# Performance work log

Measured on AMD Instinct MI355X. Metric: run time of the kernel, lower is better.

## Reference

```python
import jax, jax.numpy as jnp
import numpy as np

B = 16384
IN_DIM = 28 * 28
HID = 768
NUM_EXPERTS = 8
NUM_CLASSES = 10
H_PHASOR = 32          # phasor bank harmonics -> 2*H features
DELTA0 = 7.0
DECAY = 0.7            # spiking attention leak
THETA = 1.0
K_WINNERS = 5
TOP_K_ROUTE = 2
TRAITS = (0.6, 0.6, 0.5, 0.5, 0.4)


def setup_inputs() -> dict:
    key = jax.random.key(0)
    ks = jax.random.split(key, 16)
    s = 0.02
    return {
        "x": jax.random.normal(ks[0], (B, 28, 28), jnp.float32),
        "W_in": jax.random.normal(ks[1], (IN_DIM, HID), jnp.float32) * s,
        "b_in": jnp.zeros((HID,), jnp.float32),
        "W_ph": jax.random.normal(ks[2], (2 * H_PHASOR, HID), jnp.float32) * s,
        "b_ph": jnp.zeros((HID,), jnp.float32),
        "W_gate": jax.random.normal(ks[3], (HID, NUM_EXPERTS), jnp.float32) * s,
        "b_gate": jnp.zeros((NUM_EXPERTS,), jnp.float32),
        "W_exp": jax.random.normal(ks[4], (NUM_EXPERTS, HID, HID), jnp.float32) * s,
        "b_exp": jnp.zeros((NUM_EXPERTS, HID), jnp.float32),
        "W_th": jax.random.normal(ks[5], (HID, NUM_EXPERTS), jnp.float32) * s,
        "b_th": jnp.zeros((NUM_EXPERTS,), jnp.float32),
        "W_pm": jax.random.normal(ks[6], (5, NUM_EXPERTS), jnp.float32) * s,
        "b_pm": jnp.zeros((NUM_EXPERTS,), jnp.float32),
        "W_out": jax.random.normal(ks[7], (HID, NUM_CLASSES), jnp.float32) * s,
        "b_out": jnp.zeros((NUM_CLASSES,), jnp.float32),
    }


def reference(x, W_in, b_in, W_ph, b_ph, W_gate, b_gate, W_exp, b_exp,
              W_th, b_th, W_pm, b_pm, W_out, b_out):
    Bn = x.shape[0]
    x_flat = x.reshape((Bn, -1))
    proj = x_flat @ W_in + b_in                                  # [B, HID]

    # Phasor bank on per-sample mean activation: sin/cos at H harmonics
    x_mean = jnp.mean(proj, axis=-1)                             # [B]
    freqs = DELTA0 * jnp.arange(1, H_PHASOR + 1, dtype=proj.dtype)
    phase = x_mean[:, None] * freqs[None, :]                     # [B, H]
    feats = jnp.concatenate([jnp.sin(phase), jnp.cos(phase)], -1)  # [B, 2H]
    enhanced = proj + feats @ W_ph + b_ph                        # [B, HID]

    # Top-K index selection feeding gather/scatter spiking attention
    V = enhanced.shape[-1]
    K = min(32, V)
    topk_idx = jax.lax.top_k(enhanced, K)[1].astype(jnp.int32)   # [B, K]
    w = DECAY ** jnp.arange(K, dtype=enhanced.dtype)             # decaying drive

    def gains_fn(idx):
        v = jnp.zeros((V,), enhanced.dtype).at[idx].add(w)       # scatter-add
        vals, widx = jax.lax.top_k(v, K_WINNERS)                 # k-WTA
        return jnp.ones((V,), enhanced.dtype).at[widx].add(vals / THETA)

    gains = jax.vmap(gains_fn)(topk_idx)                         # [B, V]
    attended = enhanced * gains

    # Personality bias + thalamic bias (thalamic_scale = 1.0)
    traits = jnp.asarray(TRAITS, dtype=enhanced.dtype)
    pbias = traits @ W_pm + b_pm                                 # [E]
    thal = jnp.mean(attended, axis=0) @ W_th + b_th              # [E]

    # MoE retrieval core: gate -> top-k softmax route -> combine experts
    gate_logits = attended @ W_gate + b_gate + pbias[None] + thal[None]  # [B, E]
    gvals, gidx = jax.lax.top_k(gate_logits, TOP_K_ROUTE)        # [B, k]
    gw = jax.nn.softmax(gvals, axis=-1)                          # [B, k]
    exp_out = jnp.einsum('bh,ehd->bed', attended, W_exp) + b_exp[None]   # [B, E, HID]
    sel = jnp.take_along_axis(exp_out, gidx[:, :, None], axis=1)  # [B, k, HID]
    context = jnp.sum(gw[:, :, None] * sel, axis=1)              # [B, HID]

    return context @ W_out + b_out                               # [B, classes]
```

## Files before the change

### kernel.cpp

```cpp
#include <hip/hip_runtime.h>
#include <hip/hip_bf16.h>
#include <cstddef>

#define BATCH 16384
#define IND   784
#define HID   768
#define NEXP  8
#define KT13  13

typedef short bf16x8 __attribute__((ext_vector_type(8)));
typedef float f32x4  __attribute__((ext_vector_type(4)));
typedef unsigned short ushort_t;

#define GLD16(g, l)                                                            \
  __builtin_amdgcn_global_load_lds(                                            \
      (const __attribute__((address_space(1))) unsigned int*)(g),              \
      (__attribute__((address_space(3))) unsigned int*)(l), 16, 0, 0)

__global__ __launch_bounds__(256) void k_wtrans(const float* __restrict__ Wexp,
                                                __hip_bfloat16* __restrict__ Wt)
{
  __shared__ float tile[32][33];
  const int e = blockIdx.z;
  const int h0 = blockIdx.x * 32, d0 = blockIdx.y * 32;
  const int tx = threadIdx.x & 31, ty = threadIdx.x >> 5;
  const float* src = Wexp + ((size_t)e * HID + h0) * HID + d0;
  #pragma unroll
  for (int i = 0; i < 4; i++)
    tile[ty + 8 * i][tx] = src[(size_t)(ty + 8 * i) * HID + tx];
  __syncthreads();
  __hip_bfloat16* dst = Wt + ((size_t)e * HID + d0) * HID + h0;
  #pragma unroll
  for (int i = 0; i < 4; i++)
    dst[(size_t)(ty + 8 * i) * HID + tx] = __float2bfloat16(tile[tx][ty + 8 * i]);
}

__device__ inline ushort_t bf16_rne(float f) {
  union { float f; unsigned u; } v; v.f = f;
  unsigned r = v.u + 0x7fffu + ((v.u >> 16) & 1u);
  return (ushort_t)(r >> 16);
}
__device__ inline float bf16_to_f(ushort_t h) {
  union { unsigned u; float f; } v; v.u = ((unsigned)h) << 16;
  return v.f;
}

__global__ __launch_bounds__(256) void k_packA(const float* __restrict__ x,
                                               ushort_t* __restrict__ Ahi,
                                               ushort_t* __restrict__ Alo)
{
  const int kt = blockIdx.x, mt = blockIdx.y;
  const size_t tbase = ((size_t)mt * KT13 + kt) * 8192;
  const int kb = kt * 64;
  #pragma unroll
  for (int i = 0; i < 4; i++) {
    int id = i * 256 + threadIdx.x;
    int r = id >> 3, c = id & 7;
    int row = mt * 128 + r;
    int k0 = kb + c * 8;
    float v[8];
    if (k0 + 8 <= IND) {
      const float4* p = reinterpret_cast<const float4*>(x + (size_t)row * IND + k0);
      float4 a = p[0], b = p[1];
      v[0] = a.x; v[1] = a.y; v[2] = a.z; v[3] = a.w;
      v[4] = b.x; v[5] = b.y; v[6] = b.z; v[7] = b.w;
    } else {
      #pragma unroll
      for (int j = 0; j < 8; j++) v[j] = (k0 + j < IND) ? x[(size_t)row * IND + k0 + j] : 0.f;
    }
    ushort_t hi[8], lo[8];
    #pragma unroll
    for (int j = 0; j < 8; j++) {
      hi[j] = bf16_rne(v[j]);
      lo[j] = bf16_rne(v[j] - bf16_to_f(hi[j]));
    }
    size_t dst = tbase + (size_t)r * 64 + ((c ^ (r & 7)) * 8);
    *reinterpret_cast<uint4*>(Ahi + dst) = *reinterpret_cast<uint4*>(hi);
    *reinterpret_cast<uint4*>(Alo + dst) = *reinterpret_cast<uint4*>(lo);
  }
}

__global__ __launch_bounds__(256) void k_packB(const float* __restrict__ W,
                                               ushort_t* __restrict__ Bhi,
                                               ushort_t* __restrict__ Blo)
{
  const int kt = blockIdx.x, nt = blockIdx.y;
  const size_t tbase = ((size_t)nt * KT13 + kt) * 8192;
  const int kb = kt * 64;
  #pragma unroll
  for (int i = 0; i < 4; i++) {
    int id = i * 256 + threadIdx.x;
    int r = id >> 3, c = id & 7;
    int n = nt * 128 + r;
    int k0 = kb + c * 8;
    float v[8];
    #pragma unroll
    for (int j = 0; j < 8; j++)
      v[j] = (k0 + j < IND) ? W[(size_t)(k0 + j) * HID + n] : 0.f;
    ushort_t hi[8], lo[8];
    #pragma unroll
    for (int j = 0; j < 8; j++) {
      hi[j] = bf16_rne(v[j]);
      lo[j] = bf16_rne(v[j] - bf16_to_f(hi[j]));
    }
    size_t dst = tbase + (size_t)r * 64 + ((c ^ (r & 7)) * 8);
    *reinterpret_cast<uint4*>(Bhi + dst) = *reinterpret_cast<uint4*>(hi);
    *reinterpret_cast<uint4*>(Blo + dst) = *reinterpret_cast<uint4*>(lo);
  }
}

__global__ __launch_bounds__(256, 2) void k_proj2(const ushort_t* __restrict__ Ahi,
                                                  const ushort_t* __restrict__ Alo,
                                                  const ushort_t* __restrict__ Bhi,
                                                  const ushort_t* __restrict__ Blo,
                                                  const float* __restrict__ bias,
                                                  float* __restrict__ out)
{
  __shared__ __align__(16) ushort_t lds[4 * 8192];
  const int tid = threadIdx.x, lane = tid & 63, w = tid >> 6;
  const int mt = blockIdx.y, nt = blockIdx.x;
  const int m0 = (w >> 1) * 64, n0 = (w & 1) * 64;
  const int l15 = lane & 15, g = lane >> 4;

  f32x4 acc[4][4];
  #pragma unroll
  for (int i = 0; i < 4; i++)
    #pragma unroll
    for (int j = 0; j < 4; j++) acc[i][j] = (f32x4){0.f, 0.f, 0.f, 0.f};

  const size_t abase = (size_t)mt * KT13 * 8192;
  const size_t bbase = (size_t)nt * KT13 * 8192;

  for (int kt = 0; kt < KT13; kt++) {
    __syncthreads();
    const ushort_t* srcs[4] = { Ahi + abase + (size_t)kt * 8192,
                                Alo + abase + (size_t)kt * 8192,
                                Bhi + bbase + (size_t)kt * 8192,
                                Blo + bbase + (size_t)kt * 8192 };
    #pragma unroll
    for (int buf = 0; buf < 4; buf++) {
      #pragma unroll
      for (int i = 0; i < 4; i++) {
        int off = w * 2048 + i * 512 + lane * 8;
        GLD16(srcs[buf] + off, &lds[buf * 8192 + w * 2048 + i * 512]);
      }
    }
    asm volatile("s_waitcnt vmcnt(0)");
    __syncthreads();
    #pragma unroll
    for (int ks = 0; ks < 2; ks++) {
      bf16x8 ah[4], al[4], bh[4], bl[4];
      #pragma unroll
      for (int i = 0; i < 4; i++) {
        int ca = ((4 * ks + g) ^ (l15 & 7)) * 8;
        int ra = m0 + 16 * i + l15;
        ah[i] = *reinterpret_cast<const bf16x8*>(&lds[0 * 8192 + ra * 64 + ca]);
        al[i] = *reinterpret_cast<const bf16x8*>(&lds[1 * 8192 + ra * 64 + ca]);
        int rb = n0 + 16 * i + l15;
        bh[i] = *reinterpret_cast<const bf16x8*>(&lds[2 * 8192 + rb * 64 + ca]);
        bl[i] = *reinterpret_cast<const bf16x8*>(&lds[3 * 8192 + rb * 64 + ca]);
      }
      #pragma unroll
      for (int i = 0; i < 4; i++)
        #pragma unroll
        for (int j = 0; j < 4; j++) {
          acc[i][j] = __builtin_amdgcn_mfma_f32_16x16x32_bf16(ah[i], bh[j], acc[i][j], 0, 0, 0);
          acc[i][j] = __builtin_amdgcn_mfma_f32_16x16x32_bf16(ah[i], bl[j], acc[i][j], 0, 0, 0);
          acc[i][j] = __builtin_amdgcn_mfma_f32_16x16x32_bf16(al[i], bh[j], acc[i][j], 0, 0, 0);
        }
    }
  }
  #pragma unroll
  for (int i = 0; i < 4; i++) {
    #pragma unroll
    for (int q = 0; q < 4; q++) {
      int m = mt * 128 + m0 + 16 * i + g * 4 + q;
      #pragma unroll
      for (int j = 0; j < 4; j++) {
        int n = nt * 128 + n0 + 16 * j + l15;
        out[(size_t)m * HID + n] = acc[i][j][q] + bias[n];
      }
    }
  }
}

__global__ __launch_bounds__(256) void k_mean(const float* __restrict__ proj,
                                              float* __restrict__ means)
{
  const int t = threadIdx.x, lane = t & 63, w = t >> 6;
  const int row = blockIdx.x * 4 + w;
  const float* p = proj + (size_t)row * HID;
  float s = 0.f;
  #pragma unroll
  for (int j = 0; j < 12; j++) s += p[lane + 64 * j];
  #pragma unroll
  for (int off = 32; off; off >>= 1) s += __shfl_xor(s, off);
  if (lane == 0) means[row] = s * (1.0f / 768.0f);
}

__global__ __launch_bounds__(256) void k_phasor(const float* __restrict__ means,
                                                const float* __restrict__ Wph,
                                                const float* __restrict__ bph,
                                                float* __restrict__ enh)
{
  __shared__ float Fs[64][132];
  __shared__ float Ws[64][128];
  const int t  = threadIdx.x;
  const int bm = blockIdx.y * 128, bn = blockIdx.x * 128;
  {
    const int r = t >> 1;
    const float mn = means[bm + r];
    if ((t & 1) == 0) {
      #pragma unroll
      for (int j = 0; j < 32; j++) Fs[j][r] = sinf(mn * (7.0f * (j + 1)));
    } else {
      #pragma unroll
      for (int j = 0; j < 32; j++) Fs[32 + j][r] = cosf(mn * (7.0f * (j + 1)));
    }
  }
  #pragma unroll
  for (int i = 0; i < 8; i++) {
    int f4 = i * 256 + t;
    int k = f4 >> 5, n4 = (f4 & 31) * 4;
    *reinterpret_cast<float4*>(&Ws[k][n4]) =
        *reinterpret_cast<const float4*>(Wph + (size_t)k * HID + bn + n4);
  }
  __syncthreads();

  const int m0 = (t >> 4) * 8, n0 = (t & 15) * 8;
  float acc[8][8];
  #pragma unroll
  for (int i = 0; i < 8; i++)
    #pragma unroll
    for (int j = 0; j < 8; j++) acc[i][j] = 0.f;
  #pragma unroll 4
  for (int k = 0; k < 64; k++) {
    float a[8], b[8];
    *reinterpret_cast<float4*>(&a[0]) = *reinterpret_cast<const float4*>(&Fs[k][m0]);
    *reinterpret_cast<float4*>(&a[4]) = *reinterpret_cast<const float4*>(&Fs[k][m0 + 4]);
    *reinterpret_cast<float4*>(&b[0]) = *reinterpret_cast<const float4*>(&Ws[k][n0]);
    *reinterpret_cast<float4*>(&b[4]) = *reinterpret_cast<const float4*>(&Ws[k][n0 + 4]);
    #pragma unroll
    for (int i = 0; i < 8; i++)
      #pragma unroll
      for (int j = 0; j < 8; j++) acc[i][j] = fmaf(a[i], b[j], acc[i][j]);
  }
  float bl[8];
  #pragma unroll
  for (int j = 0; j < 8; j++) bl[j] = bph[bn + n0 + j];
  #pragma unroll
  for (int i = 0; i < 8; i++) {
    float* rowp = enh + (size_t)(bm + m0 + i) * HID + bn + n0;
    float4 p0 = *reinterpret_cast<float4*>(rowp);
    float4 p1 = *reinterpret_cast<float4*>(rowp + 4);
    p0.x += acc[i][0] + bl[0]; p0.y += acc[i][1] + bl[1];
    p0.z += acc[i][2] + bl[2]; p0.w += acc[i][3] + bl[3];
    p1.x += acc[i][4] + bl[4]; p1.y += acc[i][5] + bl[5];
    p1.z += acc[i][6] + bl[6]; p1.w += acc[i][7] + bl[7];
    *reinterpret_cast<float4*>(rowp)     = p0;
    *reinterpret_cast<float4*>(rowp + 4) = p1;
  }
}

__global__ __launch_bounds__(256) void k_attend(const float* __restrict__ enh,
                                                const float* __restrict__ Wg,
                                                __hip_bfloat16* __restrict__ attb,
                                                float* __restrict__ glog,
                                                float* __restrict__ partials)
{
  __shared__ float WgT[8][768];
  __shared__ float cs[4][768];
  const int t = threadIdx.x, lane = t & 63, w = t >> 6;
  for (int i = t; i < 768 * 8; i += 256) { int c = i >> 3, e = i & 7; WgT[e][c] = Wg[i]; }
  for (int i = t; i < 4 * 768; i += 256) cs[i / 768][i % 768] = 0.f;
  __syncthreads();

  for (int rr = 0; rr < 8; ++rr) {
    const int row = blockIdx.x * 32 + rr * 4 + w;
    const float* er = enh + (size_t)row * HID;
    float o[12], s[12];
    #pragma unroll
    for (int j = 0; j < 12; j++) { o[j] = er[lane + 64 * j]; s[j] = o[j]; }

    int wc[5];
    #pragma unroll
    for (int k = 0; k < 5; k++) {
      float v = -3.4e38f; int c = 0x7fffffff;
      #pragma unroll
      for (int j = 0; j < 12; j++)
        if (s[j] > v) { v = s[j]; c = lane + 64 * j; }
      #pragma unroll
      for (int off = 32; off; off >>= 1) {
        float ov = __shfl_xor(v, off); int oc = __shfl_xor(c, off);
        if (ov > v || (ov == v && oc < c)) { v = ov; c = oc; }
      }
      wc[k] = c;
      if (lane == (c & 63)) {
        #pragma unroll
        for (int j = 0; j < 12; j++) if (j == (c >> 6)) s[j] = -3.4e38f;
      }
    }

    float a[12];
    #pragma unroll
    for (int j = 0; j < 12; j++) a[j] = o[j];
    float wv = 1.0f;
    #pragma unroll
    for (int k = 0; k < 5; k++) {
      int c = wc[k];
      if (lane == (c & 63)) {
        #pragma unroll
        for (int j = 0; j < 12; j++) if (j == (c >> 6)) a[j] = o[j] * (1.0f + wv);
      }
      wv *= 0.7f;
    }
    #pragma unroll
    for (int j = 0; j < 12; j++)
      attb[(size_t)row * HID + lane + 64 * j] = __float2bfloat16(a[j]);
    #pragma unroll
    for (int j = 0; j < 12; j++) cs[w][lane + 64 * j] += a[j];

    float p[8];
    #pragma unroll
    for (int e = 0; e < 8; e++) p[e] = 0.f;
    #pragma unroll
    for (int j = 0; j < 12; j++) {
      int c = lane + 64 * j;
      #pragma unroll
      for (int e = 0; e < 8; e++) p[e] = fmaf(a[j], WgT[e][c], p[e]);
    }
    #pragma unroll
    for (int e = 0; e < 8; e++) {
      #pragma unroll
      for (int off = 32; off; off >>= 1) p[e] += __shfl_xor(p[e], off);
    }
    if (lane == 0) {
      #pragma unroll
      for (int e = 0; e < 8; e++) glog[(size_t)row * 8 + e] = p[e];
    }
  }
  __syncthreads();
  for (int i = t; i < 768; i += 256)
    partials[(size_t)blockIdx.x * 768 + i] = cs[0][i] + cs[1][i] + cs[2][i] + cs[3][i];
}

__global__ void k_thal(const float* __restrict__ partials,
                       const float* __restrict__ Wth, const float* __restrict__ bth,
                       const float* __restrict__ Wpm, const float* __restrict__ bpm,
                       const float* __restrict__ bgate, float* __restrict__ add8)
{
  __shared__ float cm[768];
  __shared__ float th[8];
  const int t = threadIdx.x;
  float s = 0.f;
  #pragma unroll 8
  for (int b = 0; b < 512; b++) s += partials[(size_t)b * 768 + t];
  cm[t] = s * (1.0f / 16384.0f);
  __syncthreads();
  if (t < 256) {
    int e = t >> 5, l = t & 31;
    float ps = 0.f;
    for (int c = l; c < 768; c += 32) ps = fmaf(cm[c], Wth[(size_t)c * 8 + e], ps);
    #pragma unroll
    for (int off = 16; off; off >>= 1) ps += __shfl_xor(ps, off);
    if (l == 0) th[e] = ps + bth[e];
  }
  __syncthreads();
  if (t < 8) {
    const float TR[5] = {0.6f, 0.6f, 0.5f, 0.5f, 0.4f};
    float pb = bpm[t];
    #pragma unroll
    for (int i = 0; i < 5; i++) pb = fmaf(TR[i], Wpm[i * 8 + t], pb);
    add8[t] = th[t] + pb + bgate[t];
  }
}

__global__ __launch_bounds__(256) void k_route(const float* __restrict__ glog,
                                               const float* __restrict__ add8,
                                               float* __restrict__ rw,
                                               unsigned char* __restrict__ re,
                                               int* __restrict__ counts)
{
  __shared__ float a8[8];
  __shared__ int lc[8];
  const int t = threadIdx.x;
  if (t < 8) { a8[t] = add8[t]; lc[t] = 0; }
  __syncthreads();
  const int row = blockIdx.x * 256 + t;
  const float4* gp = reinterpret_cast<const float4*>(glog + (size_t)row * 8);
  float4 g0 = gp[0], g1 = gp[1];
  float l[8] = { g0.x + a8[0], g0.y + a8[1], g0.z + a8[2], g0.w + a8[3],
                 g1.x + a8[4], g1.y + a8[5], g1.z + a8[6], g1.w + a8[7] };
  float v0 = l[0], v1 = -3.4e38f; int i0 = 0, i1 = 0;
  #pragma unroll
  for (int e = 1; e < 8; e++) {
    if (l[e] > v0)      { v1 = v0; i1 = i0; v0 = l[e]; i0 = e; }
    else if (l[e] > v1) { v1 = l[e]; i1 = e; }
  }
  float ex = expf(v1 - v0);
  float inv = 1.0f / (1.0f + ex);
  rw[row * 2] = inv; rw[row * 2 + 1] = ex * inv;
  re[row * 2] = (unsigned char)i0; re[row * 2 + 1] = (unsigned char)i1;
  atomicAdd(&lc[i0], 1); atomicAdd(&lc[i1], 1);
  __syncthreads();
  if (t < 8) atomicAdd(&counts[t], lc[t]);
}

__global__ void k_prefix(const int* __restrict__ counts, int* __restrict__ meta)
{
  if (threadIdx.x == 0) {
    int o = 0, tt = 0;
    for (int e = 0; e < 8; e++) {
      meta[e] = o; meta[9 + e] = tt; meta[19 + e] = o;
      o += counts[e]; tt += (counts[e] + 127) >> 7;
    }
    meta[8] = o; meta[17] = tt; meta[18] = tt;
  }
}

__global__ __launch_bounds__(256) void k_scatter(const unsigned char* __restrict__ re,
                                                 int* __restrict__ meta,
                                                 int* __restrict__ perm,
                                                 int* __restrict__ inv)
{
  __shared__ int lc[8], base[8];
  const int t = threadIdx.x;
  if (t < 8) lc[t] = 0;
  __syncthreads();
  const int row = blockIdx.x * 256 + t;
  const int e0 = re[row * 2], e1 = re[row * 2 + 1];
  const int p0 = atomicAdd(&lc[e0], 1);
  const int p1 = atomicAdd(&lc[e1], 1);
  __syncthreads();
  if (t < 8) base[t] = atomicAdd(&meta[19 + t], lc[t]);
  __syncthreads();
  const int s0 = base[e0] + p0;
  const int s1 = base[e1] + p1;
  perm[s0] = row * 2;     inv[row * 2]     = s0;
  perm[s1] = row * 2 + 1; inv[row * 2 + 1] = s1;
}

__global__ __launch_bounds__(256) void k_expert(const unsigned short* __restrict__ attb,
                                                const unsigned short* __restrict__ Wt,
                                                const float* __restrict__ bexp,
                                                const float* __restrict__ rw,
                                                const int* __restrict__ perm,
                                                const int* __restrict__ meta,
                                                ushort_t* __restrict__ ctxP)
{
  if ((int)blockIdx.x >= meta[18]) return;
  __shared__ __align__(16) unsigned short AsBs[2 * 128 * 64];
  __shared__ int rid[128];
  __shared__ float gws[128];
  __shared__ float bxs[128];
  unsigned short* As = AsBs;
  unsigned short* Bs = AsBs + 128 * 64;

  const int* tst = meta + 9;
  const int tb = blockIdx.x;
  int e = 0;
  #pragma unroll
  for (int i = 1; i < 8; i++) if (tb >= tst[i]) e = i;
  const int tix  = tb - tst[e];
  const int off  = meta[e];
  const int cnt  = meta[e + 1] - off;
  const int rbase = off + tix * 128;
  const int vcnt  = min(128, cnt - tix * 128);
  const int tid = threadIdx.x;
  const int nb  = blockIdx.y * 128;

  if (tid < 128) {
    if (tid < vcnt) {
      int p = perm[rbase + tid];
      rid[tid] = p >> 1; gws[tid] = rw[p];
    } else {
      rid[tid] = 0; gws[tid] = 0.f;
    }
    bxs[tid] = bexp[(size_t)e * HID + nb + tid];
  }
  __syncthreads();

  const int lane = tid & 63, w = tid >> 6;
  const int m0 = (w >> 1) * 64, n0 = (w & 1) * 64;
  const int l15 = lane & 15, g = lane >> 4;
  const unsigned short* wbase = Wt + ((size_t)e * HID + nb) * HID;

  f32x4 acc[4][4];
  #pragma unroll
  for (int i = 0; i < 4; i++)
    #pragma unroll
    for (int j = 0; j < 4; j++) acc[i][j] = (f32x4){0.f, 0.f, 0.f, 0.f};

  for (int kb = 0; kb < HID; kb += 64) {
    __syncthreads();
    #pragma unroll
    for (int i = 0; i < 4; i++) {
      int id = i * 256 + tid;
      int r = id >> 3, c = id & 7;
      int sc = (c ^ (r & 7)) * 8;
      GLD16(attb + (size_t)rid[r] * HID + kb + sc, As + (i * 256 + w * 64) * 8);
      GLD16(wbase + (size_t)r * HID + kb + sc,      Bs + (i * 256 + w * 64) * 8);
    }
    asm volatile("s_waitcnt vmcnt(0)");
    __syncthreads();
    #pragma unroll
    for (int ks = 0; ks < 2; ks++) {
      bf16x8 af[4], bfr[4];
      #pragma unroll
      for (int i = 0; i < 4; i++) {
        int ca = (((4 * ks + g) ^ (l15 & 7)) * 8);
        af[i]  = *reinterpret_cast<const bf16x8*>(As + (m0 + 16 * i + l15) * 64 + ca);
        bfr[i] = *reinterpret_cast<const bf16x8*>(Bs + (n0 + 16 * i + l15) * 64 + ca);
      }
      #pragma unroll
      for (int i = 0; i < 4; i++)
        #pragma unroll
        for (int j = 0; j < 4; j++)
          acc[i][j] = __builtin_amdgcn_mfma_f32_16x16x32_bf16(af[i], bfr[j], acc[i][j], 0, 0, 0);
    }
  }

  unsigned short* Cs = AsBs;
  __syncthreads();
  #pragma unroll
  for (int i = 0; i < 4; i++) {
    #pragma unroll
    for (int q = 0; q < 4; q++) {
      int m = m0 + 16 * i + g * 4 + q;
      float gwv = gws[m];
      #pragma unroll
      for (int j = 0; j < 4; j++) {
        int n = n0 + 16 * j + l15;
        Cs[m * 128 + n] = bf16_rne(gwv * (acc[i][j][q] + bxs[n]));
      }
    }
  }
  __syncthreads();
  #pragma unroll
  for (int c = 0; c < 8; c++) {
    int r = w * 32 + c * 4 + (lane >> 4);
    if (r < vcnt) {
      uint4 v = *reinterpret_cast<const uint4*>(Cs + r * 128 + l15 * 8);
      *reinterpret_cast<uint4*>(ctxP + (size_t)(rbase + r) * HID + nb + l15 * 8) = v;
    }
  }
}

__global__ __launch_bounds__(256) void k_out(const ushort_t* __restrict__ ctxP,
                                             const int* __restrict__ inv,
                                             const float* __restrict__ Wout,
                                             const float* __restrict__ bout,
                                             float* __restrict__ out)
{
  __shared__ float wT[10][768];
  const int t = threadIdx.x, lane = t & 63, w = t >> 6;
  for (int i = t; i < 7680; i += 256) { int cl = i / 768, d = i - cl * 768; wT[cl][d] = Wout[(size_t)d * 10 + cl]; }
  __syncthreads();
  for (int rr = 0; rr < 8; ++rr) {
    const int row = blockIdx.x * 32 + rr * 4 + w;
    const int s0 = inv[row * 2], s1 = inv[row * 2 + 1];
    const ushort_t* p0 = ctxP + (size_t)s0 * HID;
    const ushort_t* p1 = ctxP + (size_t)s1 * HID;
    float cd[12];
    #pragma unroll
    for (int j = 0; j < 12; j++)
      cd[j] = bf16_to_f(p0[lane + 64 * j]) + bf16_to_f(p1[lane + 64 * j]);
    float p[10];
    #pragma unroll
    for (int cl = 0; cl < 10; cl++) {
      float ps = 0.f;
      #pragma unroll
      for (int j = 0; j < 12; j++) ps = fmaf(cd[j], wT[cl][lane + 64 * j], ps);
      #pragma unroll
      for (int off = 32; off; off >>= 1) ps += __shfl_xor(ps, off);
      p[cl] = ps;
    }
    if (lane == 0) {
      #pragma unroll
      for (int cl = 0; cl < 10; cl++) out[(size_t)row * 10 + cl] = p[cl] + bout[cl];
    }
  }
}

extern "C" void kernel_launch(void* const* d_in, const int* in_sizes, int n_in,
                              void* d_out, int out_size, void* d_ws, size_t ws_size,
                              hipStream_t stream)
{
  const float* x     = (const float*)d_in[0];
  const float* W_in  = (const float*)d_in[1];
  const float* b_in  = (const float*)d_in[2];
  const float* W_ph  = (const float*)d_in[3];
  const float* b_ph  = (const float*)d_in[4];
  const float* W_g   = (const float*)d_in[5];
  const float* b_g   = (const float*)d_in[6];
  const float* W_exp = (const float*)d_in[7];
  const float* b_exp = (const float*)d_in[8];
  const float* W_th  = (const float*)d_in[9];
  const float* b_th  = (const float*)d_in[10];
  const float* W_pm  = (const float*)d_in[11];
  const float* b_pm  = (const float*)d_in[12];
  const float* W_out = (const float*)d_in[13];
  const float* b_out = (const float*)d_in[14];
  float* out = (float*)d_out;

  char* ws = (char*)d_ws;
  size_t off = 0;
  float* enh   = (float*)(ws + off); off += (size_t)BATCH * HID * 4;
  char*  aliasbase = ws + off;
  off += (size_t)BATCH * HID * 4;
  __hip_bfloat16* attb = (__hip_bfloat16*)(ws + off); off += (size_t)BATCH * HID * 2;
  __hip_bfloat16* Wt   = (__hip_bfloat16*)(ws + off); off += (size_t)NEXP * HID * HID * 2;
  float* glog     = (float*)(ws + off); off += (size_t)BATCH * 8 * 4;
  float* partials = (float*)(ws + off); off += (size_t)512 * 768 * 4;
  float* means    = (float*)(ws + off); off += (size_t)BATCH * 4;
  float* add8     = (float*)(ws + off); off += 256;
  float* rw       = (float*)(ws + off); off += (size_t)BATCH * 2 * 4;
  unsigned char* re = (unsigned char*)(ws + off); off += (size_t)BATCH * 2;
  int* counts = (int*)(ws + off); off += 256;
  int* meta   = (int*)(ws + off); off += 256;
  int* perm   = (int*)(ws + off); off += (size_t)BATCH * 2 * 4;
  int* invp   = (int*)(ws + off); off += (size_t)BATCH * 2 * 4;
  ushort_t* Bhi = (ushort_t*)(ws + off); off += (size_t)KT13 * 64 * HID * 2;
  ushort_t* Blo = (ushort_t*)(ws + off); off += (size_t)KT13 * 64 * HID * 2;
  ushort_t* Ahi = (ushort_t*)aliasbase;
  ushort_t* Alo = (ushort_t*)(aliasbase + (size_t)BATCH * KT13 * 64 * 2);
  ushort_t* ctxP = (ushort_t*)enh;

  hipMemsetAsync(counts, 0, 32, stream);
  k_wtrans<<<dim3(24, 24, 8), 256, 0, stream>>>(W_exp, Wt);
  k_packA <<<dim3(13, 128),   256, 0, stream>>>(x, Ahi, Alo);
  k_packB <<<dim3(13, 6),     256, 0, stream>>>(W_in, Bhi, Blo);
  k_proj2 <<<dim3(6, 128),    256, 0, stream>>>(Ahi, Alo, Bhi, Blo, b_in, enh);
  k_mean  <<<4096,            256, 0, stream>>>(enh, means);
  k_phasor<<<dim3(6, 128),    256, 0, stream>>>(means, W_ph, b_ph, enh);
  k_attend<<<512,             256, 0, stream>>>(enh, W_g, attb, glog, partials);
  k_thal  <<<1,               768, 0, stream>>>(partials, W_th, b_th, W_pm, b_pm, b_g, add8);
  k_route <<<64,              256, 0, stream>>>(glog, add8, rw, re, counts);
  k_prefix<<<1,                64, 0, stream>>>(counts, meta);
  k_scatter<<<64,             256, 0, stream>>>(re, meta, perm, invp);
  k_expert<<<dim3(264, 6),    256, 0, stream>>>((const unsigned short*)attb, (const unsigned short*)Wt,
                                                b_exp, rw, perm, meta, ctxP);
  k_out   <<<512,             256, 0, stream>>>(ctxP, invp, W_out, b_out, out);
}
```

Baseline: 340.8 us.

## Fuse row-mean into projection GEMM, drop LDS staging, double-buffer expert GEMM

The projection GEMM now reads its pre-packed, unswizzled bf16 hi/lo tiles straight from global memory into registers instead of staging them through LDS. It also uses a remapped 1D block order and emits per-row partial sums, so the separate mean kernel disappears and the phasor kernel reduces 12 partials itself. The expert GEMM gains two-stage double-buffered global-to-LDS loads, and its grid is transposed so the N tiles of one expert tile run back to back. Workspace is re-aliased so attb and Wt overlay the packed A buffers, and k_wtrans moves after the projection. Direct global fragment loads may raise memory traffic, and the aliasing requires the new launch order.

```diff
diff --git a/kernel.cpp b/kernel.cpp
--- a/kernel.cpp
+++ b/kernel.cpp
@@ -74,7 +74,7 @@
       hi[j] = bf16_rne(v[j]);
       lo[j] = bf16_rne(v[j] - bf16_to_f(hi[j]));
     }
-    size_t dst = tbase + (size_t)r * 64 + ((c ^ (r & 7)) * 8);
+    size_t dst = tbase + (size_t)r * 64 + c * 8;
     *reinterpret_cast<uint4*>(Ahi + dst) = *reinterpret_cast<uint4*>(hi);
     *reinterpret_cast<uint4*>(Alo + dst) = *reinterpret_cast<uint4*>(lo);
   }
@@ -103,22 +103,24 @@
       hi[j] = bf16_rne(v[j]);
       lo[j] = bf16_rne(v[j] - bf16_to_f(hi[j]));
     }
-    size_t dst = tbase + (size_t)r * 64 + ((c ^ (r & 7)) * 8);
+    size_t dst = tbase + (size_t)r * 64 + c * 8;
     *reinterpret_cast<uint4*>(Bhi + dst) = *reinterpret_cast<uint4*>(hi);
     *reinterpret_cast<uint4*>(Blo + dst) = *reinterpret_cast<uint4*>(lo);
   }
 }
 
-__global__ __launch_bounds__(256, 2) void k_proj2(const ushort_t* __restrict__ Ahi,
-                                                  const ushort_t* __restrict__ Alo,
-                                                  const ushort_t* __restrict__ Bhi,
-                                                  const ushort_t* __restrict__ Blo,
-                                                  const float* __restrict__ bias,
-                                                  float* __restrict__ out)
-{
-  __shared__ __align__(16) ushort_t lds[4 * 8192];
+__global__ __launch_bounds__(256) void k_proj3(const ushort_t* __restrict__ Ahi,
+                                               const ushort_t* __restrict__ Alo,
+                                               const ushort_t* __restrict__ Bhi,
+                                               const ushort_t* __restrict__ Blo,
+                                               const float* __restrict__ bias,
+                                               float* __restrict__ out,
+                                               float* __restrict__ pm)
+{
+  const int bid = blockIdx.x;
+  const int sid = (bid & 7) * 96 + (bid >> 3);
+  const int mt = sid / 6, nt = sid - 6 * mt;
   const int tid = threadIdx.x, lane = tid & 63, w = tid >> 6;
-  const int mt = blockIdx.y, nt = blockIdx.x;
   const int m0 = (w >> 1) * 64, n0 = (w & 1) * 64;
   const int l15 = lane & 15, g = lane >> 4;
 
@@ -132,44 +134,36 @@
   const size_t bbase = (size_t)nt * KT13 * 8192;
 
   for (int kt = 0; kt < KT13; kt++) {
-    __syncthreads();
-    const ushort_t* srcs[4] = { Ahi + abase + (size_t)kt * 8192,
-                                Alo + abase + (size_t)kt * 8192,
-                                Bhi + bbase + (size_t)kt * 8192,
-                                Blo + bbase + (size_t)kt * 8192 };
-    #pragma unroll
-    for (int buf = 0; buf < 4; buf++) {
+    const ushort_t* ath = Ahi + abase + (size_t)kt * 8192;
+    const ushort_t* atl = Alo + abase + (size_t)kt * 8192;
+    const ushort_t* bth = Bhi + bbase + (size_t)kt * 8192;
+    const ushort_t* btl = Blo + bbase + (size_t)kt * 8192;
+    #pragma unroll
+    for (int ks = 0; ks < 2; ks++) {
+      bf16x8 ah[4], al[4], bh[4], blv[4];
       #pragma unroll
       for (int i = 0; i < 4; i++) {
-        int off = w * 2048 + i * 512 + lane * 8;
-        GLD16(srcs[buf] + off, &lds[buf * 8192 + w * 2048 + i * 512]);
-      }
-    }
-    asm volatile("s_waitcnt vmcnt(0)");
-    __syncthreads();
-    #pragma unroll
-    for (int ks = 0; ks < 2; ks++) {
-      bf16x8 ah[4], al[4], bh[4], bl[4];
-      #pragma unroll
-      for (int i = 0; i < 4; i++) {
-        int ca = ((4 * ks + g) ^ (l15 & 7)) * 8;
-        int ra = m0 + 16 * i + l15;
-        ah[i] = *reinterpret_cast<const bf16x8*>(&lds[0 * 8192 + ra * 64 + ca]);
-        al[i] = *reinterpret_cast<const bf16x8*>(&lds[1 * 8192 + ra * 64 + ca]);
-        int rb = n0 + 16 * i + l15;
-        bh[i] = *reinterpret_cast<const bf16x8*>(&lds[2 * 8192 + rb * 64 + ca]);
-        bl[i] = *reinterpret_cast<const bf16x8*>(&lds[3 * 8192 + rb * 64 + ca]);
+        int oa = (m0 + 16 * i + l15) * 64 + (4 * ks + g) * 8;
+        ah[i]  = *reinterpret_cast<const bf16x8*>(ath + oa);
+        al[i]  = *reinterpret_cast<const bf16x8*>(atl + oa);
+        int ob = (n0 + 16 * i + l15) * 64 + (4 * ks + g) * 8;
+        bh[i]  = *reinterpret_cast<const bf16x8*>(bth + ob);
+        blv[i] = *reinterpret_cast<const bf16x8*>(btl + ob);
       }
       #pragma unroll
       for (int i = 0; i < 4; i++)
         #pragma unroll
         for (int j = 0; j < 4; j++) {
-          acc[i][j] = __builtin_amdgcn_mfma_f32_16x16x32_bf16(ah[i], bh[j], acc[i][j], 0, 0, 0);
-          acc[i][j] = __builtin_amdgcn_mfma_f32_16x16x32_bf16(ah[i], bl[j], acc[i][j], 0, 0, 0);
-          acc[i][j] = __builtin_amdgcn_mfma_f32_16x16x32_bf16(al[i], bh[j], acc[i][j], 0, 0, 0);
+          acc[i][j] = __builtin_amdgcn_mfma_f32_16x16x32_bf16(ah[i], bh[j],  acc[i][j], 0, 0, 0);
+          acc[i][j] = __builtin_amdgcn_mfma_f32_16x16x32_bf16(ah[i], blv[j], acc[i][j], 0, 0, 0);
+          acc[i][j] = __builtin_amdgcn_mfma_f32_16x16x32_bf16(al[i], bh[j],  acc[i][j], 0, 0, 0);
         }
     }
   }
+
+  float bl[4];
+  #pragma unroll
+  for (int j = 0; j < 4; j++) bl[j] = bias[nt * 128 + n0 + 16 * j + l15];
   #pragma unroll
   for (int i = 0; i < 4; i++) {
     #pragma unroll
@@ -178,38 +172,45 @@
       #pragma unroll
       for (int j = 0; j < 4; j++) {
         int n = nt * 128 + n0 + 16 * j + l15;
-        out[(size_t)m * HID + n] = acc[i][j][q] + bias[n];
+        out[(size_t)m * HID + n] = acc[i][j][q] + bl[j];
       }
     }
   }
-}
-
-__global__ __launch_bounds__(256) void k_mean(const float* __restrict__ proj,
-                                              float* __restrict__ means)
-{
-  const int t = threadIdx.x, lane = t & 63, w = t >> 6;
-  const int row = blockIdx.x * 4 + w;
-  const float* p = proj + (size_t)row * HID;
-  float s = 0.f;
-  #pragma unroll
-  for (int j = 0; j < 12; j++) s += p[lane + 64 * j];
-  #pragma unroll
-  for (int off = 32; off; off >>= 1) s += __shfl_xor(s, off);
-  if (lane == 0) means[row] = s * (1.0f / 768.0f);
-}
-
-__global__ __launch_bounds__(256) void k_phasor(const float* __restrict__ means,
+  const float blsum = bl[0] + bl[1] + bl[2] + bl[3];
+  const size_t pslot = (size_t)(nt * 2 + (w & 1)) * BATCH;
+  #pragma unroll
+  for (int i = 0; i < 4; i++) {
+    #pragma unroll
+    for (int q = 0; q < 4; q++) {
+      float s = acc[i][0][q] + acc[i][1][q] + acc[i][2][q] + acc[i][3][q] + blsum;
+      s += __shfl_xor(s, 1); s += __shfl_xor(s, 2);
+      s += __shfl_xor(s, 4); s += __shfl_xor(s, 8);
+      if (l15 == 0)
+        pm[pslot + mt * 128 + m0 + 16 * i + g * 4 + q] = s;
+    }
+  }
+}
+
+__global__ __launch_bounds__(256) void k_phasor(const float* __restrict__ pm,
                                                 const float* __restrict__ Wph,
                                                 const float* __restrict__ bph,
                                                 float* __restrict__ enh)
 {
   __shared__ float Fs[64][132];
   __shared__ float Ws[64][128];
+  __shared__ float mlds[128];
   const int t  = threadIdx.x;
   const int bm = blockIdx.y * 128, bn = blockIdx.x * 128;
+  if (t < 128) {
+    float s = 0.f;
+    #pragma unroll
+    for (int k = 0; k < 12; k++) s += pm[(size_t)k * BATCH + bm + t];
+    mlds[t] = s * (1.0f / 768.0f);
+  }
+  __syncthreads();
   {
     const int r = t >> 1;
-    const float mn = means[bm + r];
+    const float mn = mlds[r];
     if ((t & 1) == 0) {
       #pragma unroll
       for (int j = 0; j < 32; j++) Fs[j][r] = sinf(mn * (7.0f * (j + 1)));
@@ -448,16 +449,14 @@
                                                 const int* __restrict__ meta,
                                                 ushort_t* __restrict__ ctxP)
 {
-  if ((int)blockIdx.x >= meta[18]) return;
-  __shared__ __align__(16) unsigned short AsBs[2 * 128 * 64];
+  if ((int)blockIdx.y >= meta[18]) return;
+  __shared__ __align__(16) ushort_t sst[2][2][8192];
   __shared__ int rid[128];
   __shared__ float gws[128];
   __shared__ float bxs[128];
-  unsigned short* As = AsBs;
-  unsigned short* Bs = AsBs + 128 * 64;
 
   const int* tst = meta + 9;
-  const int tb = blockIdx.x;
+  const int tb = blockIdx.y;
   int e = 0;
   #pragma unroll
   for (int i = 1; i < 8; i++) if (tb >= tst[i]) e = i;
@@ -467,7 +466,7 @@
   const int rbase = off + tix * 128;
   const int vcnt  = min(128, cnt - tix * 128);
   const int tid = threadIdx.x;
-  const int nb  = blockIdx.y * 128;
+  const int nb  = blockIdx.x * 128;
 
   if (tid < 128) {
     if (tid < vcnt) {
@@ -485,24 +484,33 @@
   const int l15 = lane & 15, g = lane >> 4;
   const unsigned short* wbase = Wt + ((size_t)e * HID + nb) * HID;
 
+#define ESTAGE(kb, b)                                                          \
+  { _Pragma("unroll")                                                          \
+    for (int i = 0; i < 4; i++) {                                              \
+      int id_ = i * 256 + tid; int r_ = id_ >> 3, c_ = id_ & 7;                \
+      int sc_ = (c_ ^ (r_ & 7)) * 8;                                           \
+      GLD16(attb + (size_t)rid[r_] * HID + (kb) + sc_, &sst[b][0][(i * 256 + w * 64) * 8]); \
+      GLD16(wbase + (size_t)r_ * HID + (kb) + sc_,     &sst[b][1][(i * 256 + w * 64) * 8]); \
+    } }
+
   f32x4 acc[4][4];
   #pragma unroll
   for (int i = 0; i < 4; i++)
     #pragma unroll
     for (int j = 0; j < 4; j++) acc[i][j] = (f32x4){0.f, 0.f, 0.f, 0.f};
 
-  for (int kb = 0; kb < HID; kb += 64) {
-    __syncthreads();
-    #pragma unroll
-    for (int i = 0; i < 4; i++) {
-      int id = i * 256 + tid;
-      int r = id >> 3, c = id & 7;
-      int sc = (c ^ (r & 7)) * 8;
-      GLD16(attb + (size_t)rid[r] * HID + kb + sc, As + (i * 256 + w * 64) * 8);
-      GLD16(wbase + (size_t)r * HID + kb + sc,      Bs + (i * 256 + w * 64) * 8);
-    }
-    asm volatile("s_waitcnt vmcnt(0)");
-    __syncthreads();
+  ESTAGE(0, 0);
+  for (int t = 0; t < 12; t++) {
+    const int cb = t & 1;
+    if (t < 11) {
+      ESTAGE((t + 1) * 64, cb ^ 1);
+      asm volatile("s_waitcnt vmcnt(8)" ::: "memory");
+    } else {
+      asm volatile("s_waitcnt vmcnt(0)" ::: "memory");
+    }
+    __builtin_amdgcn_s_barrier();
+    const ushort_t* As = &sst[cb][0][0];
+    const ushort_t* Bs = &sst[cb][1][0];
     #pragma unroll
     for (int ks = 0; ks < 2; ks++) {
       bf16x8 af[4], bfr[4];
@@ -518,9 +526,11 @@
         for (int j = 0; j < 4; j++)
           acc[i][j] = __builtin_amdgcn_mfma_f32_16x16x32_bf16(af[i], bfr[j], acc[i][j], 0, 0, 0);
     }
-  }
-
-  unsigned short* Cs = AsBs;
+    __builtin_amdgcn_s_barrier();
+  }
+#undef ESTAGE
+
+  unsigned short* Cs = &sst[0][0][0];
   __syncthreads();
   #pragma unroll
   for (int i = 0; i < 4; i++) {
@@ -605,14 +615,15 @@
 
   char* ws = (char*)d_ws;
   size_t off = 0;
-  float* enh   = (float*)(ws + off); off += (size_t)BATCH * HID * 4;
-  char*  aliasbase = ws + off;
-  off += (size_t)BATCH * HID * 4;
-  __hip_bfloat16* attb = (__hip_bfloat16*)(ws + off); off += (size_t)BATCH * HID * 2;
-  __hip_bfloat16* Wt   = (__hip_bfloat16*)(ws + off); off += (size_t)NEXP * HID * HID * 2;
+  float* enh = (float*)(ws + off); off += (size_t)BATCH * HID * 4;
+  char*  r1  = ws + off;           off += (size_t)2 * BATCH * KT13 * 64 * 2;
+  ushort_t* Ahi = (ushort_t*)r1;
+  ushort_t* Alo = Ahi + (size_t)BATCH * KT13 * 64;
+  __hip_bfloat16* attb = (__hip_bfloat16*)r1;
+  __hip_bfloat16* Wt   = (__hip_bfloat16*)(r1 + (size_t)BATCH * HID * 2);
   float* glog     = (float*)(ws + off); off += (size_t)BATCH * 8 * 4;
   float* partials = (float*)(ws + off); off += (size_t)512 * 768 * 4;
-  float* means    = (float*)(ws + off); off += (size_t)BATCH * 4;
+  float* pm       = (float*)(ws + off); off += (size_t)12 * BATCH * 4;
   float* add8     = (float*)(ws + off); off += 256;
   float* rw       = (float*)(ws + off); off += (size_t)BATCH * 2 * 4;
   unsigned char* re = (unsigned char*)(ws + off); off += (size_t)BATCH * 2;
@@ -622,23 +633,20 @@
   int* invp   = (int*)(ws + off); off += (size_t)BATCH * 2 * 4;
   ushort_t* Bhi = (ushort_t*)(ws + off); off += (size_t)KT13 * 64 * HID * 2;
   ushort_t* Blo = (ushort_t*)(ws + off); off += (size_t)KT13 * 64 * HID * 2;
-  ushort_t* Ahi = (ushort_t*)aliasbase;
-  ushort_t* Alo = (ushort_t*)(aliasbase + (size_t)BATCH * KT13 * 64 * 2);
   ushort_t* ctxP = (ushort_t*)enh;
 
   hipMemsetAsync(counts, 0, 32, stream);
+  k_packB <<<dim3(13, 6),     256, 0, stream>>>(W_in, Bhi, Blo);
+  k_packA <<<dim3(13, 128),   256, 0, stream>>>(x, Ahi, Alo);
+  k_proj3 <<<768,             256, 0, stream>>>(Ahi, Alo, Bhi, Blo, b_in, enh, pm);
   k_wtrans<<<dim3(24, 24, 8), 256, 0, stream>>>(W_exp, Wt);
-  k_packA <<<dim3(13, 128),   256, 0, stream>>>(x, Ahi, Alo);
-  k_packB <<<dim3(13, 6),     256, 0, stream>>>(W_in, Bhi, Blo);
-  k_proj2 <<<dim3(6, 128),    256, 0, stream>>>(Ahi, Alo, Bhi, Blo, b_in, enh);
-  k_mean  <<<4096,            256, 0, stream>>>(enh, means);
-  k_phasor<<<dim3(6, 128),    256, 0, stream>>>(means, W_ph, b_ph, enh);
+  k_phasor<<<dim3(6, 128),    256, 0, stream>>>(pm, W_ph, b_ph, enh);
   k_attend<<<512,             256, 0, stream>>>(enh, W_g, attb, glog, partials);
   k_thal  <<<1,               768, 0, stream>>>(partials, W_th, b_th, W_pm, b_pm, b_g, add8);
   k_route <<<64,              256, 0, stream>>>(glog, add8, rw, re, counts);
   k_prefix<<<1,                64, 0, stream>>>(counts, meta);
   k_scatter<<<64,             256, 0, stream>>>(re, meta, perm, invp);
-  k_expert<<<dim3(264, 6),    256, 0, stream>>>((const unsigned short*)attb, (const unsigned short*)Wt,
+  k_expert<<<dim3(6, 264),    256, 0, stream>>>((const unsigned short*)attb, (const unsigned short*)Wt,
                                                 b_exp, rw, perm, meta, ctxP);
   k_out   <<<512,             256, 0, stream>>>(ctxP, invp, W_out, b_out, out);
 }
```

After: 465.0 us. 36.5% more time.
